# Performance work log

Measured on AMD Instinct MI355X. Metric: run time of the kernel, lower is better.

Reference implementation:

```python
import jax, jax.numpy as jnp
import numpy as np

L, D, H, T, DFF = 4, 1024, 8, 1000, 4096
HS = D // H  # 128


def _rope_cos_sin():
    # theta_i = 10000^(-2(i-1)/dim) for i in 1..dim/2 (dim = head size)
    i = jnp.arange(1, HS // 2 + 1, dtype=jnp.float32)
    theta = jnp.power(jnp.float32(10000.0), -2.0 * (i - 1.0) / HS)
    t = jnp.arange(T, dtype=jnp.float32)
    ang = t[:, None] * theta[None, :]              # (T, HS/2)
    return jnp.cos(ang), jnp.sin(ang)


def _apply_rope(x, cos, sin):
    # x: (B,H,T,HS); interpret last dim as HS/2 complex pairs and multiply by e^{i t theta}
    xs = x.reshape(*x.shape[:-1], HS // 2, 2)
    xr, xi = xs[..., 0], xs[..., 1]
    c = cos[None, None, :, :]
    s = sin[None, None, :, :]
    out_r = xr * c - xi * s
    out_i = xr * s + xi * c
    return jnp.stack([out_r, out_i], axis=-1).reshape(x.shape)


def _ln(x, g, b, eps=1e-5):
    m = jnp.mean(x, axis=-1, keepdims=True)
    v = jnp.mean((x - m) ** 2, axis=-1, keepdims=True)
    return (x - m) * jax.lax.rsqrt(v + eps) * g + b


def setup_inputs() -> dict:
    key = jax.random.key(0)
    ks = jax.random.split(key, 16)
    sc = 0.02
    inp = {
        'x':   jax.random.normal(ks[0], (8, T, D), jnp.float32),
        'Wq':  sc * jax.random.normal(ks[1], (L, D, D), jnp.float32),
        'Wk':  sc * jax.random.normal(ks[2], (L, D, D), jnp.float32),
        'Wv':  sc * jax.random.normal(ks[3], (L, D, D), jnp.float32),
        'Wpk': sc * jax.random.normal(ks[4], (L, T, T), jnp.float32),
        'bpk': jnp.zeros((L, T), jnp.float32),
        'Wpv': sc * jax.random.normal(ks[5], (L, T, T), jnp.float32),
        'bpv': jnp.zeros((L, T), jnp.float32),
        'ln1_g': jnp.ones((L, D), jnp.float32),
        'ln1_b': jnp.zeros((L, D), jnp.float32),
        'W1':  sc * jax.random.normal(ks[6], (L, DFF, D), jnp.float32),
        'b1':  jnp.zeros((L, DFF), jnp.float32),
        'W2':  sc * jax.random.normal(ks[7], (L, D, DFF), jnp.float32),
        'b2':  jnp.zeros((L, D), jnp.float32),
        'ln2_g': jnp.ones((L, D), jnp.float32),
        'ln2_b': jnp.zeros((L, D), jnp.float32),
    }
    return inp


def reference(x, Wq, Wk, Wv, Wpk, bpk, Wpv, bpv, ln1_g, ln1_b,
              W1, b1, W2, b2, ln2_g, ln2_b):
    B = x.shape[0]
    cos, sin = _rope_cos_sin()
    out = x
    for l in range(L):
        src = out
        # QKV projections (bias=False), split into heads: (B,H,T,HS)
        q = jnp.einsum('btc,dc->btd', src, Wq[l]).reshape(B, T, H, HS).transpose(0, 2, 1, 3)
        k = jnp.einsum('btc,dc->btd', src, Wk[l]).reshape(B, T, H, HS).transpose(0, 2, 1, 3)
        v = jnp.einsum('btc,dc->btd', src, Wv[l]).reshape(B, T, H, HS).transpose(0, 2, 1, 3)
        # ChunkedLinear over the SEQUENCE axis for K and V (single 1000x1000 block)
        k = jnp.einsum('bhtd,ut->bhud', k, Wpk[l]) + bpk[l][None, None, :, None]
        v = jnp.einsum('bhtd,ut->bhud', v, Wpv[l]) + bpv[l][None, None, :, None]
        # RoPE on q and k
        q = _apply_rope(q, cos, sin)
        k = _apply_rope(k, cos, sin)
        # Full (non-causal; mask is commented out in source) softmax attention
        scores = jnp.einsum('bhqd,bhkd->bhqk', q, k) / jnp.sqrt(jnp.float32(HS))
        attn = jax.nn.softmax(scores, axis=-1)
        y = jnp.einsum('bhqk,bhkd->bhqd', attn, v)
        y = y.transpose(0, 2, 1, 3).reshape(B, T, D)  # NOTE: no output proj (faithful to source)
        src = _ln(src + y, ln1_g[l], ln1_b[l])
        h = jax.nn.gelu(jnp.einsum('btd,fd->btf', src, W1[l]) + b1[l], approximate=False)
        src = _ln(src + jnp.einsum('btf,df->btd', h, W2[l]) + b2[l], ln2_g[l], ln2_b[l])
        out = src
    return out
```

## Files before the change

kernel.cpp:

```cpp
#include <hip/hip_runtime.h>
#include <cstdint>
#include <cstddef>


typedef unsigned short u16;
typedef unsigned int u32;
typedef __attribute__((ext_vector_type(8))) short s16x8;
typedef __attribute__((ext_vector_type(4))) float f32x4;

#define DEV static __device__ __forceinline__

DEV float bf2f(u16 u) { union { u32 u; float f; } v; v.u = ((u32)u) << 16; return v.f; }
DEV u16 f2bf(float f) {
  union { float f; u32 u; } v; v.f = f;
  return (u16)((v.u + 0x7fffu + ((v.u >> 16) & 1u)) >> 16);
}

#define MFMA(acc_, a_, b_) \
  asm volatile("v_mfma_f32_16x16x32_bf16 %0, %1, %2, %0" : "+v"(acc_) : "v"(a_), "v"(b_))

#define GLD16(g_, l_) \
  __builtin_amdgcn_global_load_lds((const __attribute__((address_space(1))) void*)(g_), \
                                   (__attribute__((address_space(3))) void*)(l_), 16, 0, 0)

static constexpr int T_ = 1000, D_ = 1024, H_ = 8, HS_ = 128, B_ = 8;
static constexpr int BT_ = B_ * T_;

__global__ void tab_kernel(float* __restrict__ ct, float* __restrict__ st) {
  const int id = blockIdx.x * 256 + threadIdx.x;
  const int i = id & 63, t = id >> 6;
  const float theta = powf(10000.f, -(float)i * (1.f / 64.f));
  const float ang = (float)t * theta;
  ct[id] = cosf(ang);
  st[id] = sinf(ang);
}

__global__ void convert_kernel(const float* __restrict__ in, u16* __restrict__ out, int n) {
  const int i = (blockIdx.x * 256 + threadIdx.x) * 4;
  if (i < n) {
    const float4 v = *(const float4*)(in + i);
    uint2 pk;
    pk.x = (u32)f2bf(v.x) | ((u32)f2bf(v.y) << 16);
    pk.y = (u32)f2bf(v.z) | ((u32)f2bf(v.w) << 16);
    *(uint2*)(out + i) = pk;
  }
}

__global__ __launch_bounds__(256) void transpose_kernel(const u16* __restrict__ in,
                                                        u16* __restrict__ out, int cb) {
  __shared__ u16 tile[64][72];
  const int tt = blockIdx.x, dt = blockIdx.y, b = blockIdx.z;
  const int tid = threadIdx.x;
  const int r = tid >> 2, cq = (tid & 3) << 4;
  const int t = tt * 64 + r;
#pragma unroll
  for (int v = 0; v < 2; ++v) {
    s16x8 val = {};
    if (t < T_) val = *(const s16x8*)(in + (size_t)(b * 1000 + t) * 3072 + cb + dt * 64 + cq + v * 8);
    *(s16x8*)&tile[r][cq + v * 8] = val;
  }
  __syncthreads();
  const int d = dt * 64 + r;
  u16 vals[16];
#pragma unroll
  for (int j = 0; j < 16; ++j) vals[j] = tile[cq + j][r];
  u16* o = out + (size_t)b * 1048576 + (size_t)d * 1024 + tt * 64 + cq;
  *(s16x8*)o = *(s16x8*)&vals[0];
  *(s16x8*)(o + 8) = *(s16x8*)&vals[8];
}

template <int BIAS, bool ACT, bool OUTBF>
__global__ __launch_bounds__(256) void gemm2p(
    const u16* __restrict__ A, const u16* __restrict__ B, void* __restrict__ Cv,
    const float* __restrict__ bias, int M, int N, int K, int lda, int ldb, int ldc,
    long sA, long sB, long sC) {
  __shared__ alignas(16) u16 As[2][4096];
  __shared__ alignas(16) u16 Bs[2][4096];
  const int z = blockIdx.z;
  A += (size_t)z * (size_t)sA;
  B += (size_t)z * (size_t)sB;
  const int m0 = blockIdx.y * 128, n0 = blockIdx.x * 128;
  const int tid = threadIdx.x;
  const int wid = tid >> 6, lane = tid & 63;
  const int wr = wid >> 1, wc = wid & 1;
  const int l15 = lane & 15, l4 = lane >> 4;
  const int srow = tid >> 2;
  const int sg = ((tid & 3) ^ ((tid >> 3) & 3)) << 3;
  const u16* gA0 = A + (size_t)min(m0 + srow, M - 1) * lda + sg;
  const u16* gA1 = A + (size_t)min(m0 + 64 + srow, M - 1) * lda + sg;
  const u16* gB0 = B + (size_t)min(n0 + srow, N - 1) * ldb + sg;
  const u16* gB1 = B + (size_t)min(n0 + 64 + srow, N - 1) * ldb + sg;
  const int gg = (l4 ^ ((l15 >> 1) & 3)) << 3;
  const int aBase = (wr * 64 + l15) * 32 + gg;
  const int bBase = (wc * 64 + l15) * 32 + gg;

  f32x4 acc[4][4] = {};
  const int KT = K >> 5;
  GLD16(gA0, &As[0][tid * 8]);
  GLD16(gA1, &As[0][(256 + tid) * 8]);
  GLD16(gB0, &Bs[0][tid * 8]);
  GLD16(gB1, &Bs[0][(256 + tid) * 8]);
  __syncthreads();
  int cur = 0;
#pragma unroll 1
  for (int kt = 0; kt < KT; ++kt) {
    if (kt + 1 < KT) {
      const int kb = (kt + 1) << 5;
      GLD16(gA0 + kb, &As[cur ^ 1][tid * 8]);
      GLD16(gA1 + kb, &As[cur ^ 1][(256 + tid) * 8]);
      GLD16(gB0 + kb, &Bs[cur ^ 1][tid * 8]);
      GLD16(gB1 + kb, &Bs[cur ^ 1][(256 + tid) * 8]);
    }
    s16x8 af[4], bfr[4];
#pragma unroll
    for (int i = 0; i < 4; ++i) af[i] = *(const s16x8*)&As[cur][aBase + i * 512];
#pragma unroll
    for (int i = 0; i < 4; ++i) bfr[i] = *(const s16x8*)&Bs[cur][bBase + i * 512];
    __builtin_amdgcn_s_setprio(1);
#pragma unroll
    for (int mi = 0; mi < 4; ++mi)
#pragma unroll
      for (int ni = 0; ni < 4; ++ni) MFMA(acc[mi][ni], af[mi], bfr[ni]);
    __builtin_amdgcn_s_setprio(0);
    __syncthreads();
    cur ^= 1;
  }
  asm volatile("s_nop 7\n\ts_nop 7"
               : "+v"(acc[3][0]), "+v"(acc[3][1]), "+v"(acc[3][2]), "+v"(acc[3][3]));
#pragma unroll
  for (int mi = 0; mi < 4; ++mi) {
#pragma unroll
    for (int ni = 0; ni < 4; ++ni) {
      const int colg = n0 + wc * 64 + ni * 16 + l15;
#pragma unroll
      for (int r = 0; r < 4; ++r) {
        const int rowg = m0 + wr * 64 + mi * 16 + l4 * 4 + r;
        if (rowg < M && colg < N) {
          float v = acc[mi][ni][r];
          if (BIAS == 1) v += bias[rowg];
          if (BIAS == 2) v += bias[colg];
          if (ACT) v = 0.5f * v * (1.0f + erff(v * 0.70710678118654752f));
          const size_t idx = (size_t)z * (size_t)sC + (size_t)rowg * ldc + colg;
          if (OUTBF) ((u16*)Cv)[idx] = f2bf(v);
          else       ((float*)Cv)[idx] = v;
        }
      }
    }
  }
}

__global__ __launch_bounds__(256) void rope_kernel(u16* __restrict__ X, int ld,
                                                   const float* __restrict__ ct,
                                                   const float* __restrict__ st) {
  const int id = blockIdx.x * 256 + threadIdx.x;
  const int i = id & 63;
  const int h = (id >> 6) & 7;
  const int bt = id >> 9;
  const int t = bt % 1000;
  const size_t base = (size_t)bt * ld + h * HS_ + i * 2;
  u32* p = (u32*)(X + base);
  const u32 w = *p;
  const float xr = bf2f((u16)(w & 0xffffu));
  const float xi = bf2f((u16)(w >> 16));
  const float c = ct[t * 64 + i], s = st[t * 64 + i];
  const float outr = xr * c - xi * s;
  const float outi = xr * s + xi * c;
  *p = (u32)f2bf(outr) | ((u32)f2bf(outi) << 16);
}

__global__ __launch_bounds__(256) void attn_kernel(const u16* __restrict__ Q, int ldq,
                                                   const u16* __restrict__ Km,
                                                   const u16* __restrict__ Vmt,
                                                   float* __restrict__ Y) {
  __shared__ alignas(16) u16 Ks[64][136];
  __shared__ alignas(16) u16 Vts[128][72];
  __shared__ alignas(16) u16 Ps[4][32][72];
  const int qt = blockIdx.x;
  const int bh = blockIdx.y;
  const int b = bh >> 3, h = bh & 7;
  const int tid = threadIdx.x;
  const int w = tid >> 6, lane = tid & 63;
  const int l15 = lane & 15, l4 = lane >> 4;
  const size_t qbase = (size_t)b * 1000 * ldq + h * HS_;
  const size_t kbase = (size_t)b * 1024000 + h * HS_;
  const size_t vbase = (size_t)b * 1048576 + (size_t)(h * HS_) * 1024;
  const int q0 = qt * 128 + w * 32;
  s16x8 aq[2][4];
#pragma unroll
  for (int qf = 0; qf < 2; ++qf) {
    const int qrow = q0 + qf * 16 + l15;
#pragma unroll
    for (int c = 0; c < 4; ++c) {
      s16x8 v = {};
      if (qrow < T_) v = *(const s16x8*)(Q + qbase + (size_t)qrow * ldq + c * 32 + l4 * 8);
      aq[qf][c] = v;
    }
  }
  f32x4 acc[2][8] = {};
  float m_run[2][4], l_run[2][4];
#pragma unroll
  for (int qf = 0; qf < 2; ++qf)
#pragma unroll
    for (int r = 0; r < 4; ++r) { m_run[qf][r] = -1e30f; l_run[qf][r] = 0.f; }
  const float SCALE = 0.08838834764831845f;
  for (int kt = 0; kt < 16; ++kt) {
    {
      const int r = tid >> 2, c0 = (tid & 3) << 5;
      const int kk = kt * 64 + r;
#pragma unroll
      for (int v = 0; v < 4; ++v) {
        s16x8 val = {};
        if (kk < T_) val = *(const s16x8*)(Km + kbase + (size_t)kk * 1024 + c0 + v * 8);
        *(s16x8*)&Ks[r][c0 + v * 8] = val;
      }
      const int r2 = tid >> 1, c2s = (tid & 1) << 5;
#pragma unroll
      for (int v = 0; v < 4; ++v) {
        const s16x8 val = *(const s16x8*)(Vmt + vbase + (size_t)r2 * 1024 + kt * 64 + c2s + v * 8);
        *(s16x8*)&Vts[r2][c2s + v * 8] = val;
      }
    }
    __syncthreads();
    f32x4 sacc[2][4] = {};
#pragma unroll
    for (int c = 0; c < 4; ++c) {
      s16x8 bk[4];
#pragma unroll
      for (int f = 0; f < 4; ++f) bk[f] = *(const s16x8*)&Ks[f * 16 + l15][c * 32 + l4 * 8];
#pragma unroll
      for (int qf = 0; qf < 2; ++qf)
#pragma unroll
        for (int f = 0; f < 4; ++f) MFMA(sacc[qf][f], aq[qf][c], bk[f]);
    }
    asm volatile("s_nop 7\n\ts_nop 7"
                 : "+v"(sacc[0][0]), "+v"(sacc[0][1]), "+v"(sacc[0][2]), "+v"(sacc[0][3]),
                   "+v"(sacc[1][0]), "+v"(sacc[1][1]), "+v"(sacc[1][2]), "+v"(sacc[1][3]));
#pragma unroll
    for (int qf = 0; qf < 2; ++qf) {
      float sv[4][4];
#pragma unroll
      for (int f = 0; f < 4; ++f) {
        const int key = kt * 64 + f * 16 + l15;
#pragma unroll
        for (int r = 0; r < 4; ++r) sv[f][r] = (key < T_) ? sacc[qf][f][r] * SCALE : -1e30f;
      }
#pragma unroll
      for (int r = 0; r < 4; ++r) {
        float mx = fmaxf(fmaxf(sv[0][r], sv[1][r]), fmaxf(sv[2][r], sv[3][r]));
#pragma unroll
        for (int off = 8; off >= 1; off >>= 1) mx = fmaxf(mx, __shfl_xor(mx, off));
        const float mn = fmaxf(m_run[qf][r], mx);
        const float corr = __expf(m_run[qf][r] - mn);
        m_run[qf][r] = mn;
        float rs = 0.f;
#pragma unroll
        for (int f = 0; f < 4; ++f) {
          const float p = __expf(sv[f][r] - mn);
          rs += p;
          Ps[w][qf * 16 + l4 * 4 + r][f * 16 + l15] = f2bf(p);
        }
#pragma unroll
        for (int off = 8; off >= 1; off >>= 1) rs += __shfl_xor(rs, off);
        l_run[qf][r] = l_run[qf][r] * corr + rs;
#pragma unroll
        for (int n = 0; n < 8; ++n) acc[qf][n][r] *= corr;
      }
    }
    asm volatile("s_waitcnt lgkmcnt(0)" ::: "memory");
#pragma unroll
    for (int c2 = 0; c2 < 2; ++c2) {
      s16x8 pa[2];
#pragma unroll
      for (int qf = 0; qf < 2; ++qf)
        pa[qf] = *(const s16x8*)&Ps[w][qf * 16 + l15][c2 * 32 + l4 * 8];
#pragma unroll
      for (int n = 0; n < 8; ++n) {
        const s16x8 vb = *(const s16x8*)&Vts[n * 16 + l15][c2 * 32 + l4 * 8];
#pragma unroll
        for (int qf = 0; qf < 2; ++qf) MFMA(acc[qf][n], pa[qf], vb);
      }
    }
    __syncthreads();
  }
  asm volatile("s_nop 7\n\ts_nop 7"
               : "+v"(acc[0][6]), "+v"(acc[0][7]), "+v"(acc[1][6]), "+v"(acc[1][7]));
#pragma unroll
  for (int qf = 0; qf < 2; ++qf)
#pragma unroll
    for (int n = 0; n < 8; ++n)
#pragma unroll
      for (int r = 0; r < 4; ++r) {
        const int q = q0 + qf * 16 + l4 * 4 + r;
        if (q < T_)
          Y[(size_t)(b * 1000 + q) * 1024 + h * HS_ + n * 16 + l15] = acc[qf][n][r] / l_run[qf][r];
      }
}

__global__ __launch_bounds__(256) void addln_kernel(float* __restrict__ src,
                                                    const float* __restrict__ add,
                                                    const float* __restrict__ g,
                                                    const float* __restrict__ bb,
                                                    u16* __restrict__ outb) {
  const int row = blockIdx.x;
  const int tid = threadIdx.x;
  float* s = src + (size_t)row * D_;
  const float* a = add + (size_t)row * D_;
  float x[4];
  float sum = 0.f, sq = 0.f;
#pragma unroll
  for (int i = 0; i < 4; ++i) {
    const int d = tid + i * 256;
    const float v = s[d] + a[d];
    x[i] = v; sum += v; sq += v * v;
  }
#pragma unroll
  for (int off = 32; off >= 1; off >>= 1) { sum += __shfl_xor(sum, off); sq += __shfl_xor(sq, off); }
  __shared__ float red[8];
  const int wid = tid >> 6;
  if ((tid & 63) == 0) { red[wid] = sum; red[4 + wid] = sq; }
  __syncthreads();
  sum = red[0] + red[1] + red[2] + red[3];
  sq = red[4] + red[5] + red[6] + red[7];
  const float mean = sum * (1.f / 1024.f);
  const float var = sq * (1.f / 1024.f) - mean * mean;
  const float rstd = rsqrtf(var + 1e-5f);
#pragma unroll
  for (int i = 0; i < 4; ++i) {
    const int d = tid + i * 256;
    const float y = (x[i] - mean) * rstd * g[d] + bb[d];
    s[d] = y;
    outb[(size_t)row * D_ + d] = f2bf(y);
  }
}

static inline int cdiv(int a, int b) { return (a + b - 1) / b; }

extern "C" void kernel_launch(void* const* d_in, const int* in_sizes, int n_in,
                              void* d_out, int out_size, void* d_ws, size_t ws_size,
                              hipStream_t stream) {
  const float* x    = (const float*)d_in[0];
  const float* Wq   = (const float*)d_in[1];
  const float* Wk   = (const float*)d_in[2];
  const float* Wv   = (const float*)d_in[3];
  const float* Wpk  = (const float*)d_in[4];
  const float* bpk  = (const float*)d_in[5];
  const float* Wpv  = (const float*)d_in[6];
  const float* bpv  = (const float*)d_in[7];
  const float* g1   = (const float*)d_in[8];
  const float* b1ln = (const float*)d_in[9];
  const float* W1   = (const float*)d_in[10];
  const float* b1   = (const float*)d_in[11];
  const float* W2   = (const float*)d_in[12];
  const float* b2   = (const float*)d_in[13];
  const float* g2   = (const float*)d_in[14];
  const float* b2ln = (const float*)d_in[15];

  char* wsb = (char*)d_ws;
  float* cosT = (float*)(wsb + 0);
  float* sinT = (float*)(wsb + 262144);
  float* srcf = (float*)(wsb + 524288);
  u16* srcb   = (u16*)(wsb + 33292288);
  u16* QKVb   = (u16*)(wsb + 49676288);
  u16* Ttmp   = (u16*)(wsb + 98828288);
  u16* Km     = (u16*)(wsb + 115605504);
  u16* Vmt    = (u16*)(wsb + 131989504);
  u16* wbuf   = (u16*)(wsb + 148766720);
  u16* hB     = QKVb;

  u16* wqB  = wbuf + 0;
  u16* wpkB = wbuf + 3145728;
  u16* wpvB = wbuf + 4145728;
  u16* w1B  = wbuf + 5145728;
  u16* w2B  = wbuf + 9340032;

  float* yF = (float*)d_out;

  tab_kernel<<<250, 256, 0, stream>>>(cosT, sinT);
  hipMemcpyAsync(srcf, x, (size_t)BT_ * D_ * sizeof(float), hipMemcpyDeviceToDevice, stream);
  convert_kernel<<<cdiv(BT_ * D_, 1024), 256, 0, stream>>>(x, srcb, BT_ * D_);

  for (int l = 0; l < 4; ++l) {
    convert_kernel<<<cdiv(1048576, 1024), 256, 0, stream>>>(Wq + (size_t)l * 1048576, wqB, 1048576);
    convert_kernel<<<cdiv(1048576, 1024), 256, 0, stream>>>(Wk + (size_t)l * 1048576, wqB + 1048576, 1048576);
    convert_kernel<<<cdiv(1048576, 1024), 256, 0, stream>>>(Wv + (size_t)l * 1048576, wqB + 2097152, 1048576);
    convert_kernel<<<cdiv(1000000, 1024), 256, 0, stream>>>(Wpk + (size_t)l * 1000000, wpkB, 1000000);
    convert_kernel<<<cdiv(1000000, 1024), 256, 0, stream>>>(Wpv + (size_t)l * 1000000, wpvB, 1000000);
    convert_kernel<<<cdiv(4194304, 1024), 256, 0, stream>>>(W1 + (size_t)l * 4194304, w1B, 4194304);
    convert_kernel<<<cdiv(4194304, 1024), 256, 0, stream>>>(W2 + (size_t)l * 4194304, w2B, 4194304);

    gemm2p<0, false, true><<<dim3(24, 63, 1), 256, 0, stream>>>(
        srcb, wqB, QKVb, nullptr, BT_, 3072, 1024, 1024, 1024, 3072, 0, 0, 0);

    transpose_kernel<<<dim3(16, 16, 8), 256, 0, stream>>>(QKVb, Ttmp, 1024);
    gemm2p<1, false, true><<<dim3(8, 8, 8), 256, 0, stream>>>(
        wpkB, Ttmp, Km, bpk + (size_t)l * 1000, 1000, 1024, 1024,
        1000, 1024, 1024, 0L, 1048576L, 1024000L);

    transpose_kernel<<<dim3(16, 16, 8), 256, 0, stream>>>(QKVb, Ttmp, 2048);
    gemm2p<2, false, true><<<dim3(8, 8, 8), 256, 0, stream>>>(
        Ttmp, wpvB, Vmt, bpv + (size_t)l * 1000, 1024, 1000, 1024,
        1024, 1000, 1024, 1048576L, 0L, 1048576L);

    rope_kernel<<<16000, 256, 0, stream>>>(QKVb, 3072, cosT, sinT);
    rope_kernel<<<16000, 256, 0, stream>>>(Km, 1024, cosT, sinT);

    attn_kernel<<<dim3(8, 64), 256, 0, stream>>>(QKVb, 3072, Km, Vmt, yF);

    addln_kernel<<<BT_, 256, 0, stream>>>(srcf, yF, g1 + (size_t)l * 1024,
                                          b1ln + (size_t)l * 1024, srcb);

    gemm2p<2, true, true><<<dim3(32, 63, 1), 256, 0, stream>>>(
        srcb, w1B, hB, b1 + (size_t)l * 4096, BT_, 4096, 1024, 1024, 1024, 4096, 0, 0, 0);
    gemm2p<2, false, false><<<dim3(8, 63, 1), 256, 0, stream>>>(
        hB, w2B, d_out, b2 + (size_t)l * 1024, BT_, 1024, 4096, 4096, 4096, 1024, 0, 0, 0);

    addln_kernel<<<BT_, 256, 0, stream>>>(srcf, yF, g2 + (size_t)l * 1024,
                                          b2ln + (size_t)l * 1024, srcb);
  }

  hipMemcpyAsync(d_out, srcf, (size_t)BT_ * D_ * sizeof(float), hipMemcpyDeviceToDevice, stream);
}
```

Before: 2.286 ms.

## Fuse K/V transpose into QKV GEMM epilogue, RoPE into attention, bf16 intermediates

```diff
diff --git a/kernel.cpp b/kernel.cpp
--- a/kernel.cpp
+++ b/kernel.cpp
@@ -7,6 +7,7 @@
 typedef unsigned int u32;
 typedef __attribute__((ext_vector_type(8))) short s16x8;
 typedef __attribute__((ext_vector_type(4))) float f32x4;
+typedef __attribute__((ext_vector_type(4))) unsigned short u16x4;
 
 #define DEV static __device__ __forceinline__
 
@@ -25,6 +26,18 @@
 
 static constexpr int T_ = 1000, D_ = 1024, H_ = 8, HS_ = 128, B_ = 8;
 static constexpr int BT_ = B_ * T_;
+
+DEV void rope8(s16x8& v, const float* __restrict__ ct, const float* __restrict__ st,
+               int t, int i0) {
+  const f32x4 c4 = *(const f32x4*)(ct + t * 64 + i0);
+  const f32x4 s4 = *(const f32x4*)(st + t * 64 + i0);
+#pragma unroll
+  for (int p = 0; p < 4; ++p) {
+    const float xr = bf2f((u16)v[2 * p]), xi = bf2f((u16)v[2 * p + 1]);
+    v[2 * p]     = (short)f2bf(xr * c4[p] - xi * s4[p]);
+    v[2 * p + 1] = (short)f2bf(xr * s4[p] + xi * c4[p]);
+  }
+}
 
 __global__ void tab_kernel(float* __restrict__ ct, float* __restrict__ st) {
   const int id = blockIdx.x * 256 + threadIdx.x;
@@ -46,34 +59,21 @@
   }
 }
 
-__global__ __launch_bounds__(256) void transpose_kernel(const u16* __restrict__ in,
-                                                        u16* __restrict__ out, int cb) {
-  __shared__ u16 tile[64][72];
-  const int tt = blockIdx.x, dt = blockIdx.y, b = blockIdx.z;
-  const int tid = threadIdx.x;
-  const int r = tid >> 2, cq = (tid & 3) << 4;
-  const int t = tt * 64 + r;
-#pragma unroll
-  for (int v = 0; v < 2; ++v) {
-    s16x8 val = {};
-    if (t < T_) val = *(const s16x8*)(in + (size_t)(b * 1000 + t) * 3072 + cb + dt * 64 + cq + v * 8);
-    *(s16x8*)&tile[r][cq + v * 8] = val;
-  }
-  __syncthreads();
-  const int d = dt * 64 + r;
-  u16 vals[16];
-#pragma unroll
-  for (int j = 0; j < 16; ++j) vals[j] = tile[cq + j][r];
-  u16* o = out + (size_t)b * 1048576 + (size_t)d * 1024 + tt * 64 + cq;
-  *(s16x8*)o = *(s16x8*)&vals[0];
-  *(s16x8*)(o + 8) = *(s16x8*)&vals[8];
-}
-
-template <int BIAS, bool ACT, bool OUTBF>
+__global__ void zerotail_kernel(u16* __restrict__ KTg, u16* __restrict__ VTg,
+                                u16* __restrict__ Vmt) {
+  const int id = blockIdx.x * 256 + threadIdx.x;
+  if (id >= 3 * 8192 * 24) return;
+  const int which = id / 196608, rem = id % 196608;
+  const int bd = rem / 24, t = 1000 + rem % 24;
+  u16* p = (which == 0) ? KTg : (which == 1) ? VTg : Vmt;
+  p[(size_t)bd * 1024 + t] = 0;
+}
+
+template <int BIAS, bool ACT, bool OUTBF, bool SPLIT>
 __global__ __launch_bounds__(256) void gemm2p(
     const u16* __restrict__ A, const u16* __restrict__ B, void* __restrict__ Cv,
-    const float* __restrict__ bias, int M, int N, int K, int lda, int ldb, int ldc,
-    long sA, long sB, long sC) {
+    const float* __restrict__ bias, u16* __restrict__ KT, u16* __restrict__ VT,
+    int M, int N, int K, int lda, int ldb, int ldc, long sA, long sB, long sC) {
   __shared__ alignas(16) u16 As[2][4096];
   __shared__ alignas(16) u16 Bs[2][4096];
   const int z = blockIdx.z;
@@ -95,7 +95,7 @@
   const int bBase = (wc * 64 + l15) * 32 + gg;
 
   f32x4 acc[4][4] = {};
-  const int KT = K >> 5;
+  const int KT_n = K >> 5;
   GLD16(gA0, &As[0][tid * 8]);
   GLD16(gA1, &As[0][(256 + tid) * 8]);
   GLD16(gB0, &Bs[0][tid * 8]);
@@ -103,8 +103,8 @@
   __syncthreads();
   int cur = 0;
 #pragma unroll 1
-  for (int kt = 0; kt < KT; ++kt) {
-    if (kt + 1 < KT) {
+  for (int kt = 0; kt < KT_n; ++kt) {
+    if (kt + 1 < KT_n) {
       const int kb = (kt + 1) << 5;
       GLD16(gA0 + kb, &As[cur ^ 1][tid * 8]);
       GLD16(gA1 + kb, &As[cur ^ 1][(256 + tid) * 8]);
@@ -127,51 +127,61 @@
   }
   asm volatile("s_nop 7\n\ts_nop 7"
                : "+v"(acc[3][0]), "+v"(acc[3][1]), "+v"(acc[3][2]), "+v"(acc[3][3]));
-#pragma unroll
-  for (int mi = 0; mi < 4; ++mi) {
-#pragma unroll
-    for (int ni = 0; ni < 4; ++ni) {
-      const int colg = n0 + wc * 64 + ni * 16 + l15;
-#pragma unroll
-      for (int r = 0; r < 4; ++r) {
-        const int rowg = m0 + wr * 64 + mi * 16 + l4 * 4 + r;
-        if (rowg < M && colg < N) {
-          float v = acc[mi][ni][r];
-          if (BIAS == 1) v += bias[rowg];
-          if (BIAS == 2) v += bias[colg];
-          if (ACT) v = 0.5f * v * (1.0f + erff(v * 0.70710678118654752f));
-          const size_t idx = (size_t)z * (size_t)sC + (size_t)rowg * ldc + colg;
-          if (OUTBF) ((u16*)Cv)[idx] = f2bf(v);
-          else       ((float*)Cv)[idx] = v;
+  if constexpr (SPLIT) {
+#pragma unroll
+    for (int mi = 0; mi < 4; ++mi) {
+      const int rb = m0 + wr * 64 + mi * 16 + l4 * 4;
+      if (rb < M) {
+#pragma unroll
+        for (int ni = 0; ni < 4; ++ni) {
+          const int colg = n0 + wc * 64 + ni * 16 + l15;
+          if (colg < 1024) {
+#pragma unroll
+            for (int r = 0; r < 4; ++r)
+              ((u16*)Cv)[(size_t)(rb + r) * 1024 + colg] = f2bf(acc[mi][ni][r]);
+          } else {
+            u16* dst = (colg < 2048) ? KT : VT;
+            const int dcol = colg & 1023;
+            const int bq = rb / 1000;
+            const int tq = rb - bq * 1000;
+            u16x4 pk;
+#pragma unroll
+            for (int r = 0; r < 4; ++r) pk[r] = f2bf(acc[mi][ni][r]);
+            *(u16x4*)(dst + (size_t)bq * 1048576 + (size_t)dcol * 1024 + tq) = pk;
+          }
         }
       }
     }
-  }
-}
-
-__global__ __launch_bounds__(256) void rope_kernel(u16* __restrict__ X, int ld,
+  } else {
+#pragma unroll
+    for (int mi = 0; mi < 4; ++mi) {
+#pragma unroll
+      for (int ni = 0; ni < 4; ++ni) {
+        const int colg = n0 + wc * 64 + ni * 16 + l15;
+#pragma unroll
+        for (int r = 0; r < 4; ++r) {
+          const int rowg = m0 + wr * 64 + mi * 16 + l4 * 4 + r;
+          if (rowg < M && colg < N) {
+            float v = acc[mi][ni][r];
+            if (BIAS == 1) v += bias[rowg];
+            if (BIAS == 2) v += bias[colg];
+            if (ACT) v = 0.5f * v * (1.0f + erff(v * 0.70710678118654752f));
+            const size_t idx = (size_t)z * (size_t)sC + (size_t)rowg * ldc + colg;
+            if (OUTBF) ((u16*)Cv)[idx] = f2bf(v);
+            else       ((float*)Cv)[idx] = v;
+          }
+        }
+      }
+    }
+  }
+}
+
+__global__ __launch_bounds__(256) void attn_kernel(const u16* __restrict__ Q,
+                                                   const u16* __restrict__ Km,
+                                                   const u16* __restrict__ Vmt,
+                                                   u16* __restrict__ Y,
                                                    const float* __restrict__ ct,
                                                    const float* __restrict__ st) {
-  const int id = blockIdx.x * 256 + threadIdx.x;
-  const int i = id & 63;
-  const int h = (id >> 6) & 7;
-  const int bt = id >> 9;
-  const int t = bt % 1000;
-  const size_t base = (size_t)bt * ld + h * HS_ + i * 2;
-  u32* p = (u32*)(X + base);
-  const u32 w = *p;
-  const float xr = bf2f((u16)(w & 0xffffu));
-  const float xi = bf2f((u16)(w >> 16));
-  const float c = ct[t * 64 + i], s = st[t * 64 + i];
-  const float outr = xr * c - xi * s;
-  const float outi = xr * s + xi * c;
-  *p = (u32)f2bf(outr) | ((u32)f2bf(outi) << 16);
-}
-
-__global__ __launch_bounds__(256) void attn_kernel(const u16* __restrict__ Q, int ldq,
-                                                   const u16* __restrict__ Km,
-                                                   const u16* __restrict__ Vmt,
-                                                   float* __restrict__ Y) {
   __shared__ alignas(16) u16 Ks[64][136];
   __shared__ alignas(16) u16 Vts[128][72];
   __shared__ alignas(16) u16 Ps[4][32][72];
@@ -181,7 +191,7 @@
   const int tid = threadIdx.x;
   const int w = tid >> 6, lane = tid & 63;
   const int l15 = lane & 15, l4 = lane >> 4;
-  const size_t qbase = (size_t)b * 1000 * ldq + h * HS_;
+  const size_t qbase = (size_t)b * 1000 * 1024 + h * HS_;
   const size_t kbase = (size_t)b * 1024000 + h * HS_;
   const size_t vbase = (size_t)b * 1048576 + (size_t)(h * HS_) * 1024;
   const int q0 = qt * 128 + w * 32;
@@ -192,7 +202,10 @@
 #pragma unroll
     for (int c = 0; c < 4; ++c) {
       s16x8 v = {};
-      if (qrow < T_) v = *(const s16x8*)(Q + qbase + (size_t)qrow * ldq + c * 32 + l4 * 8);
+      if (qrow < T_) {
+        v = *(const s16x8*)(Q + qbase + (size_t)qrow * 1024 + c * 32 + l4 * 8);
+        rope8(v, ct, st, qrow, c * 16 + l4 * 4);
+      }
       aq[qf][c] = v;
     }
   }
@@ -210,7 +223,10 @@
 #pragma unroll
       for (int v = 0; v < 4; ++v) {
         s16x8 val = {};
-        if (kk < T_) val = *(const s16x8*)(Km + kbase + (size_t)kk * 1024 + c0 + v * 8);
+        if (kk < T_) {
+          val = *(const s16x8*)(Km + kbase + (size_t)kk * 1024 + c0 + v * 8);
+          rope8(val, ct, st, kk, (c0 + v * 8) >> 1);
+        }
         *(s16x8*)&Ks[r][c0 + v * 8] = val;
       }
       const int r2 = tid >> 1, c2s = (tid & 1) << 5;
@@ -292,25 +308,28 @@
       for (int r = 0; r < 4; ++r) {
         const int q = q0 + qf * 16 + l4 * 4 + r;
         if (q < T_)
-          Y[(size_t)(b * 1000 + q) * 1024 + h * HS_ + n * 16 + l15] = acc[qf][n][r] / l_run[qf][r];
+          Y[(size_t)(b * 1000 + q) * 1024 + h * HS_ + n * 16 + l15] =
+              f2bf(acc[qf][n][r] / l_run[qf][r]);
       }
 }
 
 __global__ __launch_bounds__(256) void addln_kernel(float* __restrict__ src,
-                                                    const float* __restrict__ add,
+                                                    const u16* __restrict__ add,
                                                     const float* __restrict__ g,
                                                     const float* __restrict__ bb,
                                                     u16* __restrict__ outb) {
   const int row = blockIdx.x;
   const int tid = threadIdx.x;
+  const int d = tid * 4;
   float* s = src + (size_t)row * D_;
-  const float* a = add + (size_t)row * D_;
+  const u16* a = add + (size_t)row * D_;
+  f32x4 sv = *(const f32x4*)(s + d);
+  const u16x4 av = *(const u16x4*)(a + d);
   float x[4];
   float sum = 0.f, sq = 0.f;
 #pragma unroll
   for (int i = 0; i < 4; ++i) {
-    const int d = tid + i * 256;
-    const float v = s[d] + a[d];
+    const float v = sv[i] + bf2f(av[i]);
     x[i] = v; sum += v; sq += v * v;
   }
 #pragma unroll
@@ -324,13 +343,18 @@
   const float mean = sum * (1.f / 1024.f);
   const float var = sq * (1.f / 1024.f) - mean * mean;
   const float rstd = rsqrtf(var + 1e-5f);
+  const f32x4 gv = *(const f32x4*)(g + d);
+  const f32x4 bv = *(const f32x4*)(bb + d);
+  f32x4 yv;
+  u16x4 ob;
 #pragma unroll
   for (int i = 0; i < 4; ++i) {
-    const int d = tid + i * 256;
-    const float y = (x[i] - mean) * rstd * g[d] + bb[d];
-    s[d] = y;
-    outb[(size_t)row * D_ + d] = f2bf(y);
-  }
+    const float y = (x[i] - mean) * rstd * gv[i] + bv[i];
+    yv[i] = y;
+    ob[i] = f2bf(y);
+  }
+  *(f32x4*)(s + d) = yv;
+  *(u16x4*)(outb + (size_t)row * D_ + d) = ob;
 }
 
 static inline int cdiv(int a, int b) { return (a + b - 1) / b; }
@@ -360,12 +384,14 @@
   float* sinT = (float*)(wsb + 262144);
   float* srcf = (float*)(wsb + 524288);
   u16* srcb   = (u16*)(wsb + 33292288);
-  u16* QKVb   = (u16*)(wsb + 49676288);
-  u16* Ttmp   = (u16*)(wsb + 98828288);
-  u16* Km     = (u16*)(wsb + 115605504);
-  u16* Vmt    = (u16*)(wsb + 131989504);
-  u16* wbuf   = (u16*)(wsb + 148766720);
-  u16* hB     = QKVb;
+  u16* Qb     = (u16*)(wsb + 49676288);
+  u16* KTg    = (u16*)(wsb + 66060288);
+  u16* VTg    = (u16*)(wsb + 82837504);
+  u16* Km     = (u16*)(wsb + 99614720);
+  u16* Vmt    = (u16*)(wsb + 115998720);
+  u16* yB     = (u16*)(wsb + 132775936);
+  u16* wbuf   = (u16*)(wsb + 149159936);
+  u16* hB     = Qb;
 
   u16* wqB  = wbuf + 0;
   u16* wpkB = wbuf + 3145728;
@@ -373,9 +399,8 @@
   u16* w1B  = wbuf + 5145728;
   u16* w2B  = wbuf + 9340032;
 
-  float* yF = (float*)d_out;
-
   tab_kernel<<<250, 256, 0, stream>>>(cosT, sinT);
+  zerotail_kernel<<<2304, 256, 0, stream>>>(KTg, VTg, Vmt);
   hipMemcpyAsync(srcf, x, (size_t)BT_ * D_ * sizeof(float), hipMemcpyDeviceToDevice, stream);
   convert_kernel<<<cdiv(BT_ * D_, 1024), 256, 0, stream>>>(x, srcb, BT_ * D_);
 
@@ -388,33 +413,30 @@
     convert_kernel<<<cdiv(4194304, 1024), 256, 0, stream>>>(W1 + (size_t)l * 4194304, w1B, 4194304);
     convert_kernel<<<cdiv(4194304, 1024), 256, 0, stream>>>(W2 + (size_t)l * 4194304, w2B, 4194304);
 
-    gemm2p<0, false, true><<<dim3(24, 63, 1), 256, 0, stream>>>(
-        srcb, wqB, QKVb, nullptr, BT_, 3072, 1024, 1024, 1024, 3072, 0, 0, 0);
-
-    transpose_kernel<<<dim3(16, 16, 8), 256, 0, stream>>>(QKVb, Ttmp, 1024);
-    gemm2p<1, false, true><<<dim3(8, 8, 8), 256, 0, stream>>>(
-        wpkB, Ttmp, Km, bpk + (size_t)l * 1000, 1000, 1024, 1024,
-        1000, 1024, 1024, 0L, 1048576L, 1024000L);
-
-    transpose_kernel<<<dim3(16, 16, 8), 256, 0, stream>>>(QKVb, Ttmp, 2048);
-    gemm2p<2, false, true><<<dim3(8, 8, 8), 256, 0, stream>>>(
-        Ttmp, wpvB, Vmt, bpv + (size_t)l * 1000, 1024, 1000, 1024,
-        1024, 1000, 1024, 1048576L, 0L, 1048576L);
-
-    rope_kernel<<<16000, 256, 0, stream>>>(QKVb, 3072, cosT, sinT);
-    rope_kernel<<<16000, 256, 0, stream>>>(Km, 1024, cosT, sinT);
-
-    attn_kernel<<<dim3(8, 64), 256, 0, stream>>>(QKVb, 3072, Km, Vmt, yF);
-
-    addln_kernel<<<BT_, 256, 0, stream>>>(srcf, yF, g1 + (size_t)l * 1024,
+    gemm2p<0, false, true, true><<<dim3(24, 63, 1), 256, 0, stream>>>(
+        srcb, wqB, Qb, nullptr, KTg, VTg, BT_, 3072, 1024, 1024, 1024, 1024, 0, 0, 0);
+
+    gemm2p<1, false, true, false><<<dim3(8, 8, 8), 256, 0, stream>>>(
+        wpkB, KTg, Km, bpk + (size_t)l * 1000, nullptr, nullptr,
+        1000, 1024, 1024, 1000, 1024, 1024, 0L, 1048576L, 1024000L);
+
+    gemm2p<2, false, true, false><<<dim3(8, 8, 8), 256, 0, stream>>>(
+        VTg, wpvB, Vmt, bpv + (size_t)l * 1000, nullptr, nullptr,
+        1024, 1000, 1024, 1024, 1000, 1024, 1048576L, 0L, 1048576L);
+
+    attn_kernel<<<dim3(8, 64), 256, 0, stream>>>(Qb, Km, Vmt, yB, cosT, sinT);
+
+    addln_kernel<<<BT_, 256, 0, stream>>>(srcf, yB, g1 + (size_t)l * 1024,
                                           b1ln + (size_t)l * 1024, srcb);
 
-    gemm2p<2, true, true><<<dim3(32, 63, 1), 256, 0, stream>>>(
-        srcb, w1B, hB, b1 + (size_t)l * 4096, BT_, 4096, 1024, 1024, 1024, 4096, 0, 0, 0);
-    gemm2p<2, false, false><<<dim3(8, 63, 1), 256, 0, stream>>>(
-        hB, w2B, d_out, b2 + (size_t)l * 1024, BT_, 1024, 4096, 4096, 4096, 1024, 0, 0, 0);
-
-    addln_kernel<<<BT_, 256, 0, stream>>>(srcf, yF, g2 + (size_t)l * 1024,
+    gemm2p<2, true, true, false><<<dim3(32, 63, 1), 256, 0, stream>>>(
+        srcb, w1B, hB, b1 + (size_t)l * 4096, nullptr, nullptr,
+        BT_, 4096, 1024, 1024, 1024, 4096, 0, 0, 0);
+    gemm2p<2, false, true, false><<<dim3(8, 63, 1), 256, 0, stream>>>(
+        hB, w2B, yB, b2 + (size_t)l * 1024, nullptr, nullptr,
+        BT_, 1024, 4096, 4096, 4096, 1024, 0, 0, 0);
+
+    addln_kernel<<<BT_, 256, 0, stream>>>(srcf, yB, g2 + (size_t)l * 1024,
                                           b2ln + (size_t)l * 1024, srcb);
   }
 
```

Result: faster. 2.205 ms (-3.5%).
